# Kernel tuning notes

Hardware: AMD Instinct MI355X
Metric: run time of the kernel (lower is better)

## Reference

```python
import jax, jax.numpy as jnp
import numpy as np
from jax import lax

WS = 7            # window size
DIM = 256         # out_dim
HEADS = 8
HD = DIM // HEADS # head dim = 32
HIDDEN = 4 * DIM  # mlp hidden = 1024
IN_DIM = 512
EPS = 1e-6

def _rel_pos_index(ws):
    coords = np.stack(np.meshgrid(np.arange(ws), np.arange(ws), indexing='ij'))
    cf = coords.reshape(2, -1)
    rc = (cf[:, :, None] - cf[:, None, :]).transpose(1, 2, 0)
    rc[:, :, 0] += ws - 1
    rc[:, :, 1] += ws - 1
    rc[:, :, 0] *= 2 * ws - 1
    return rc.sum(-1)  # (N, N)

RPI = jnp.asarray(_rel_pos_index(WS))  # (49, 49) int

def _layernorm(x, g, b):
    m = jnp.mean(x, axis=-1, keepdims=True)
    v = jnp.mean(jnp.square(x - m), axis=-1, keepdims=True)
    return (x - m) * lax.rsqrt(v + EPS) * g + b

def setup_inputs() -> dict:
    key = jax.random.key(0)
    ks = jax.random.split(key, 16)
    s = 0.02
    inp = {
        'x': jax.random.normal(ks[0], (8, IN_DIM, 48, 48), jnp.float32),
        'skip_feat': jax.random.normal(ks[1], (8, DIM, 96, 96), jnp.float32),
        # ConvTranspose2d(in, out, k=2, s=2): weight (in, out, 2, 2), bias (out,)
        'up_w': jax.random.normal(ks[2], (IN_DIM, DIM, 2, 2), jnp.float32) * s,
        'up_b': jnp.zeros((DIM,), jnp.float32),
        # skip_adapter Conv2d(out, out, 1, bias=False)
        'skip_w': jax.random.normal(ks[3], (DIM, DIM, 1, 1), jnp.float32) * s,
        'gamma1': jnp.ones((DIM,), jnp.float32),
        'beta1': jnp.zeros((DIM,), jnp.float32),
        'qkv_w': jax.random.normal(ks[4], (3 * DIM, DIM), jnp.float32) * s,
        'qkv_b': jnp.zeros((3 * DIM,), jnp.float32),
        'rpb_table': jax.random.normal(ks[5], ((2 * WS - 1) ** 2, HEADS), jnp.float32) * s,
        'proj_w': jax.random.normal(ks[6], (DIM, DIM), jnp.float32) * s,
        'proj_b': jnp.zeros((DIM,), jnp.float32),
        'gamma2': jnp.ones((DIM,), jnp.float32),
        'beta2': jnp.zeros((DIM,), jnp.float32),
        'mlp_w1': jax.random.normal(ks[7], (HIDDEN, DIM), jnp.float32) * s,
        'mlp_b1': jnp.zeros((HIDDEN,), jnp.float32),
        'mlp_w2': jax.random.normal(ks[8], (DIM, HIDDEN), jnp.float32) * s,
        'mlp_b2': jnp.zeros((DIM,), jnp.float32),
    }
    return inp

def _forward(x, skip_feat, up_w, up_b, skip_w, gamma1, beta1, qkv_w, qkv_b,
             rpb_table, proj_w, proj_b, gamma2, beta2, mlp_w1, mlp_b1, mlp_w2, mlp_b2):
    B = x.shape[0]
    # ConvTranspose2d k=2 s=2 p=0 == lhs-dilated conv with spatially flipped kernel
    y = lax.conv_general_dilated(
        x, jnp.flip(up_w, (2, 3)), window_strides=(1, 1),
        padding=((1, 1), (1, 1)), lhs_dilation=(2, 2),
        dimension_numbers=('NCHW', 'IOHW', 'NCHW')) + up_b[None, :, None, None]
    shortcut = y  # (B, C, Hup, Wup)
    # skip adapter (1x1 conv, no bias); shapes match so no interpolate/adhoc conv
    y = y + jnp.einsum('oi,bihw->bohw', skip_w[:, :, 0, 0], skip_feat)
    xh = jnp.transpose(y, (0, 2, 3, 1))  # (B, H, W, C)
    H, W, C = xh.shape[1], xh.shape[2], xh.shape[3]
    xn = _layernorm(xh, gamma1, beta1)
    pad_b = (WS - H % WS) % WS
    pad_r = (WS - W % WS) % WS
    xp = jnp.pad(xn, ((0, 0), (0, pad_b), (0, pad_r), (0, 0)))
    Hp, Wp = H + pad_b, W + pad_r
    N = WS * WS
    # window partition -> (B * nWh * nWw, N, C)
    win = xp.reshape(B, Hp // WS, WS, Wp // WS, WS, C)
    win = jnp.transpose(win, (0, 1, 3, 2, 4, 5)).reshape(-1, N, C)
    B_ = win.shape[0]
    # attention
    qkv = (win @ qkv_w.T + qkv_b).reshape(B_, N, 3, HEADS, HD)
    qkv = jnp.transpose(qkv, (2, 0, 3, 1, 4))  # (3, B_, h, N, hd)
    q, k, v = qkv[0], qkv[1], qkv[2]
    attn = jnp.einsum('bhnd,bhmd->bhnm', q * (HD ** -0.5), k)
    bias = rpb_table[RPI.reshape(-1)].reshape(N, N, HEADS)
    attn = attn + jnp.transpose(bias, (2, 0, 1))[None]  # (B_, h, N, N)
    attn = jax.nn.softmax(attn, axis=-1)
    o = jnp.einsum('bhnm,bhmd->bhnd', attn, v)
    o = jnp.transpose(o, (0, 2, 1, 3)).reshape(B_, N, C)
    o = o @ proj_w.T + proj_b
    # window reverse + crop
    o = o.reshape(B, Hp // WS, Wp // WS, WS, WS, C)
    o = jnp.transpose(o, (0, 1, 3, 2, 4, 5)).reshape(B, Hp, Wp, C)[:, :H, :W]
    x2 = jnp.transpose(shortcut, (0, 2, 3, 1)) + o
    # MLP
    h = jax.nn.gelu(_layernorm(x2, gamma2, beta2) @ mlp_w1.T + mlp_b1, approximate=False)
    x3 = x2 + (h @ mlp_w2.T + mlp_b2)
    return jnp.transpose(x3, (0, 3, 1, 2))  # (B, C, Hup, Wup)

def reference(x, skip_feat, up_w, up_b, skip_w, gamma1, beta1, qkv_w, qkv_b,
              rpb_table, proj_w, proj_b, gamma2, beta2, mlp_w1, mlp_b1, mlp_w2, mlp_b2):
    return _forward(x, skip_feat, up_w, up_b, skip_w, gamma1, beta1, qkv_w, qkv_b,
                    rpb_table, proj_w, proj_b, gamma2, beta2, mlp_w1, mlp_b1, mlp_w2, mlp_b2)
```

## Files before the change

kernel.cpp:

```cpp
#include <hip/hip_runtime.h>

typedef __attribute__((ext_vector_type(8))) short short8;
typedef __attribute__((ext_vector_type(4))) float f32x4;
typedef __attribute__((ext_vector_type(4))) unsigned short u16x4;
typedef unsigned short u16;
typedef unsigned int u32;

#define DEV static __device__ __forceinline__

DEV u16 f2b(float f) {
  u32 u = __builtin_bit_cast(u32, f);
  return (u16)((u + 0x7fffu + ((u >> 16) & 1u)) >> 16);
}
DEV float b2f(u16 h) {
  u32 u = ((u32)h) << 16;
  return __builtin_bit_cast(float, u);
}
DEV short8 ld8(const u16* p) { return *reinterpret_cast<const short8*>(p); }
DEV f32x4 mfma16(short8 a, short8 b, f32x4 c) {
  return __builtin_amdgcn_mfma_f32_16x16x32_bf16(a, b, c, 0, 0, 0);
}
DEV float wredsum(float v) {
#pragma unroll
  for (int off = 1; off < 64; off <<= 1) v += __shfl_xor(v, off);
  return v;
}

#define GLL(gp, lp) __builtin_amdgcn_global_load_lds( \
    (const __attribute__((address_space(1))) void*)(gp), \
    (__attribute__((address_space(3))) void*)(lp), 16, 0, 0)

#define WQKV   0
#define WPROJ  196608
#define WM1    262144
#define WM2    524288
#define WSKIP  786432
#define WUP    851968

#define OFF_BIAS 2752512u
#define OFF_SC   2883584u
#define OFF_OVR  40632320u
#define OFF_STAT (OFF_OVR + 52000000u)
#define OFF_PST  (OFF_OVR + 52600000u)
#define OFF_SGB  (OFF_OVR + 55000000u)
#define WS_NEED  96227328u

__global__ void k_sentinel(float* out) { out[threadIdx.x] = 31337.0f; }

__global__ __launch_bounds__(256) void k_prep(
    const float* qkv_w, const float* proj_w, const float* mlp_w1,
    const float* mlp_w2, const float* skip_w, const float* up_w,
    const float* rpb, const float* g1, const float* be1,
    const float* g2, const float* be2, u16* W, float* bias_g, float* sgb) {
  int i = blockIdx.x * 256 + threadIdx.x;
  if (i < 196608) { W[WQKV + i] = f2b(qkv_w[i] * g1[i & 255]); return; }
  i -= 196608;
  if (i < 65536) { W[WPROJ + i] = f2b(proj_w[i]); return; }
  i -= 65536;
  if (i < 262144) { W[WM1 + i] = f2b(mlp_w1[i] * g2[i & 255]); return; }
  i -= 262144;
  if (i < 262144) { W[WM2 + i] = f2b(mlp_w2[i]); return; }
  i -= 262144;
  if (i < 65536) { W[WSKIP + i] = f2b(skip_w[i]); return; }
  i -= 65536;
  if (i < 524288) {
    int ci = i & 511; int rest = i >> 9; int co = rest & 255; int kk = rest >> 8;
    W[WUP + i] = f2b(up_w[ci * 1024 + co * 4 + kk]);
    return;
  }
  i -= 524288;
  if (i < 32768) {
    int h = i >> 12, r = i & 4095, ii = r >> 6, j = r & 63;
    float v;
    if (j >= 49) v = -1e30f;
    else if (ii >= 49) v = 0.f;
    else {
      int d0 = (ii / 7 - j / 7) + 6, d1 = (ii % 7 - j % 7) + 6;
      v = rpb[(d0 * 13 + d1) * 8 + h];
    }
    bias_g[i] = v;
    return;
  }
  i -= 32768;
  if (i < 1024) {
    float s = 0.f;
    for (int k = 0; k < 256; k++) s += g2[k] * mlp_w1[i * 256 + k];
    sgb[i] = s;
    return;
  }
  i -= 1024;
  if (i < 1024) {
    float s = 0.f;
    for (int k = 0; k < 256; k++) s += be2[k] * mlp_w1[i * 256 + k];
    sgb[1024 + i] = s;
    return;
  }
  i -= 1024;
  if (i < 768) {
    float s = 0.f;
    for (int k = 0; k < 256; k++) s += be1[k] * qkv_w[i * 256 + k];
    sgb[2816 + i] = s;
    return;
  }
}

__global__ __launch_bounds__(256) void k_tr(const float* src, u16* dst, int C, int HW) {
  __shared__ float t[32][33];
  int hw0 = blockIdx.x * 32, c0 = blockIdx.y * 32, b = blockIdx.z;
  int tx = threadIdx.x & 31, ty = threadIdx.x >> 5;
  const float* s = src + (size_t)b * C * HW;
  u16* d = dst + (size_t)b * C * HW;
#pragma unroll
  for (int i = 0; i < 4; i++)
    t[ty + i * 8][tx] = s[(size_t)(c0 + ty + i * 8) * HW + hw0 + tx];
  __syncthreads();
#pragma unroll
  for (int i = 0; i < 4; i++)
    d[(size_t)(hw0 + ty + i * 8) * C + c0 + tx] = f2b(t[tx][ty + i * 8]);
}

__global__ __launch_bounds__(256) void k_tr_skip(const float* src, u16* dst) {
  __shared__ float t[32][33];
  int w0 = blockIdx.x * 32, c0 = blockIdx.y * 32;
  int z = blockIdx.z;
  int b = z / 96, h = z - b * 96;
  int tx = threadIdx.x & 31, ty = threadIdx.x >> 5;
  const float* s = src + (size_t)b * 256 * 9216 + (size_t)h * 96;
  u16* d = dst + (((size_t)b * 96 + h) * 96) * 256;
#pragma unroll
  for (int i = 0; i < 4; i++)
    t[ty + i * 8][tx] = s[(size_t)(c0 + ty + i * 8) * 9216 + w0 + tx];
  __syncthreads();
#pragma unroll
  for (int i = 0; i < 4; i++)
    d[(size_t)(w0 + ty + i * 8) * 256 + c0 + tx] = f2b(t[tx][ty + i * 8]);
}

__global__ __launch_bounds__(256) void k1g(
    const u16* W, const u16* xt, const float* up_b, u16* sc) {
  __shared__ __align__(16) u16 Ab[2][4096];
  __shared__ __align__(16) u16 Bb[2][4096];
  int tid = threadIdx.x;
  int lane = tid & 63, wave = tid >> 6;
  int m = lane & 15, gq = lane >> 4;
  int wr = wave >> 1, wc = wave & 1;
  int bm = blockIdx.x * 128, bn = blockIdx.y * 128;
  int kk = blockIdx.z, kh = kk >> 1, kw = kk & 1;
  const u16* Ag = xt + (size_t)bm * 512;
  const u16* Bg = W + WUP + (size_t)kk * 131072 + (size_t)bn * 512;
  f32x4 acc[4][4] = {};
#pragma unroll
  for (int c = 0; c < 2; c++) {
    int flat = (wave * 2 + c) * 512 + lane * 8;
    int r = flat >> 5, cc = flat & 31;
    GLL(Ag + (size_t)r * 512 + cc, &Ab[0][(wave * 2 + c) * 512]);
    GLL(Bg + (size_t)r * 512 + cc, &Bb[0][(wave * 2 + c) * 512]);
  }
  __syncthreads();
  int cur = 0;
  for (int ki = 0; ki < 16; ki++) {
    if (ki < 15) {
      int kkk = (ki + 1) * 32;
#pragma unroll
      for (int c = 0; c < 2; c++) {
        int flat = (wave * 2 + c) * 512 + lane * 8;
        int r = flat >> 5, cc = flat & 31;
        GLL(Ag + (size_t)r * 512 + kkk + cc, &Ab[cur ^ 1][(wave * 2 + c) * 512]);
        GLL(Bg + (size_t)r * 512 + kkk + cc, &Bb[cur ^ 1][(wave * 2 + c) * 512]);
      }
    }
    short8 aF[4], bF[4];
#pragma unroll
    for (int mt = 0; mt < 4; mt++)
      aF[mt] = ld8(&Ab[cur][(wr * 64 + mt * 16 + m) * 32 + gq * 8]);
#pragma unroll
    for (int nt = 0; nt < 4; nt++)
      bF[nt] = ld8(&Bb[cur][(wc * 64 + nt * 16 + m) * 32 + gq * 8]);
#pragma unroll
    for (int mt = 0; mt < 4; mt++)
#pragma unroll
      for (int nt = 0; nt < 4; nt++)
        acc[mt][nt] = mfma16(aF[mt], bF[nt], acc[mt][nt]);
    __syncthreads();
    cur ^= 1;
  }
  float ub[4];
#pragma unroll
  for (int nt = 0; nt < 4; nt++) ub[nt] = up_b[bn + wc * 64 + nt * 16 + m];
#pragma unroll
  for (int mt = 0; mt < 4; mt++)
#pragma unroll
    for (int rr = 0; rr < 4; rr++) {
      int t = bm + wr * 64 + mt * 16 + gq * 4 + rr;
      int b = t / 2304, rem = t - b * 2304;
      int ih = rem / 48, iw = rem - ih * 48;
      int h = 2 * ih + kh, w = 2 * iw + kw;
      size_t tok = ((size_t)b * 96 + h) * 96 + w;
#pragma unroll
      for (int nt = 0; nt < 4; nt++) {
        int ch = bn + wc * 64 + nt * 16 + m;
        sc[tok * 256 + ch] = f2b(acc[mt][nt][rr] + ub[nt]);
      }
    }
}

__global__ __launch_bounds__(256) void k2y(
    const u16* W, const u16* skt, const u16* sc, u16* ybuf, float* pstat) {
  __shared__ __align__(16) u16 Ab[2][4096];
  __shared__ __align__(16) u16 Bb[2][4096];
  int tid = threadIdx.x;
  int lane = tid & 63, wave = tid >> 6;
  int m = lane & 15, gq = lane >> 4;
  int wr = wave >> 1, wc = wave & 1;
  int bm = blockIdx.x * 128, bn = blockIdx.y * 128;
  const u16* Ag = skt + (size_t)bm * 256;
  const u16* Bg = W + WSKIP + (size_t)bn * 256;
  f32x4 acc[4][4] = {};
#pragma unroll
  for (int c = 0; c < 2; c++) {
    int flat = (wave * 2 + c) * 512 + lane * 8;
    int r = flat >> 5, cc = flat & 31;
    GLL(Ag + (size_t)r * 256 + cc, &Ab[0][(wave * 2 + c) * 512]);
    GLL(Bg + (size_t)r * 256 + cc, &Bb[0][(wave * 2 + c) * 512]);
  }
  __syncthreads();
  int cur = 0;
  for (int ki = 0; ki < 8; ki++) {
    if (ki < 7) {
      int kk = (ki + 1) * 32;
#pragma unroll
      for (int c = 0; c < 2; c++) {
        int flat = (wave * 2 + c) * 512 + lane * 8;
        int r = flat >> 5, cc = flat & 31;
        GLL(Ag + (size_t)r * 256 + kk + cc, &Ab[cur ^ 1][(wave * 2 + c) * 512]);
        GLL(Bg + (size_t)r * 256 + kk + cc, &Bb[cur ^ 1][(wave * 2 + c) * 512]);
      }
    }
    short8 aF[4], bF[4];
#pragma unroll
    for (int mt = 0; mt < 4; mt++)
      aF[mt] = ld8(&Ab[cur][(wr * 64 + mt * 16 + m) * 32 + gq * 8]);
#pragma unroll
    for (int nt = 0; nt < 4; nt++)
      bF[nt] = ld8(&Bb[cur][(wc * 64 + nt * 16 + m) * 32 + gq * 8]);
#pragma unroll
    for (int mt = 0; mt < 4; mt++)
#pragma unroll
      for (int nt = 0; nt < 4; nt++)
        acc[mt][nt] = mfma16(aF[mt], bF[nt], acc[mt][nt]);
    __syncthreads();
    cur ^= 1;
  }
#pragma unroll
  for (int mt = 0; mt < 4; mt++)
#pragma unroll
    for (int rr = 0; rr < 4; rr++) {
      int tok = bm + wr * 64 + mt * 16 + gq * 4 + rr;
      float s = 0.f, s2 = 0.f;
#pragma unroll
      for (int nt = 0; nt < 4; nt++) {
        int ch = bn + wc * 64 + nt * 16 + m;
        float y = acc[mt][nt][rr] + b2f(sc[(size_t)tok * 256 + ch]);
        ybuf[(size_t)tok * 256 + ch] = f2b(y);
        s += y; s2 += y * y;
      }
#pragma unroll
      for (int off = 1; off < 16; off <<= 1) {
        s += __shfl_xor(s, off);
        s2 += __shfl_xor(s2, off);
      }
      if (m == 0) {
        int pi = (tok * 4 + blockIdx.y * 2 + wc) * 2;
        pstat[pi] = s;
        pstat[pi + 1] = s2;
      }
    }
}

__global__ __launch_bounds__(256) void k_statfin(const float* pstat, float* stat) {
  int row = blockIdx.x * 256 + threadIdx.x;
  float s = 0.f, s2 = 0.f;
#pragma unroll
  for (int j = 0; j < 4; j++) {
    s += pstat[(row * 4 + j) * 2];
    s2 += pstat[(row * 4 + j) * 2 + 1];
  }
  float mean = s * 0.00390625f;
  float var = s2 * 0.00390625f - mean * mean;
  float r = rsqrtf(var + 1e-6f);
  stat[row * 2] = r;
  stat[row * 2 + 1] = r * mean;
}

__global__ __launch_bounds__(256) void k23(
    const u16* W, const u16* ybuf, const float* stat, const float* sgb,
    const float* qkv_b, const float* bias_g, u16* obr) {
  __shared__ __align__(16) u16 yl[52 * 264];
  __shared__ __align__(16) u16 pws[4][6144];
  int tid = threadIdx.x;
  int lane = tid & 63, wave = tid >> 6;
  int m = lane & 15, gq = lane >> 4, k0 = gq * 8;
  int blk = blockIdx.x;
  int bimg = blk / 196, wl = blk - bimg * 196;
  int wrow = wl / 14, wcol = wl - wrow * 14;
  int h0 = wrow * 7, w0 = wcol * 7;
  u16* prv = pws[wave];
#pragma unroll
  for (int t = 0; t < 8; t++) {
    u16x4 z = {};
    *reinterpret_cast<u16x4*>(&prv[t * 256 + lane * 4]) = z;
  }
  for (int it = 0; it < 7; it++) {
    int flat = it * 256 + tid;
    if (flat < 1568) {
      int row = flat >> 5, cc = (flat & 31) * 8;
      int hh = h0 + row / 7, ww = w0 + row % 7;
      short8 v = {};
      if (hh < 96 && ww < 96) {
        int ras = (bimg * 96 + hh) * 96 + ww;
        short8 raw = ld8(ybuf + (size_t)ras * 256 + cc);
        float rs = stat[ras * 2], rmu = stat[ras * 2 + 1];
#pragma unroll
        for (int q2 = 0; q2 < 8; q2++) {
          float zz = b2f(((const u16*)&raw)[q2]) * rs - rmu;
          ((u16*)&v)[q2] = f2b(zz);
        }
      }
      *reinterpret_cast<short8*>(&yl[row * 264 + cc]) = v;
    }
  }
  __syncthreads();
  const float scale = 0.1767766952966369f;
#pragma unroll
  for (int hp = 0; hp < 2; hp++) {
    int h = wave * 2 + hp;
    {
      f32x4 acc[4][6] = {};
#pragma unroll 2
      for (int ks = 0; ks < 8; ks++) {
        short8 a[4];
#pragma unroll
        for (int mt = 0; mt < 4; mt++) {
          int row = mt * 16 + m; if (row > 48) row = 48;
          a[mt] = ld8(&yl[row * 264 + ks * 32 + k0]);
        }
#pragma unroll
        for (int nt = 0; nt < 6; nt++) {
          int brow = (nt >> 1) * 256 + h * 32 + (nt & 1) * 16 + m;
          short8 bb = ld8(W + WQKV + (size_t)brow * 256 + ks * 32 + k0);
#pragma unroll
          for (int mt = 0; mt < 4; mt++)
            acc[mt][nt] = mfma16(a[mt], bb, acc[mt][nt]);
        }
      }
      float qb_[6], sb1[6];
      int hdv[6];
#pragma unroll
      for (int nt = 0; nt < 6; nt++) {
        int hd = (nt & 1) * 16 + m;
        int c = (nt >> 1) * 256 + h * 32 + hd;
        qb_[nt] = qkv_b[c];
        sb1[nt] = sgb[2816 + c];
        hdv[nt] = hd;
      }
#pragma unroll
      for (int mt = 0; mt < 4; mt++)
#pragma unroll
        for (int rr = 0; rr < 4; rr++) {
          int row = mt * 16 + gq * 4 + rr;
          if (row >= 49) continue;
          int hh = h0 + row / 7, ww = w0 + row % 7;
          float vf = (hh < 96 && ww < 96) ? 1.f : 0.f;
#pragma unroll
          for (int nt = 0; nt < 6; nt++) {
            u16 val = f2b(acc[mt][nt][rr] + vf * sb1[nt] + qb_[nt]);
            if ((nt >> 1) == 0) prv[2048 + row * 32 + hdv[nt]] = val;
            else if ((nt >> 1) == 1) prv[3616 + row * 32 + hdv[nt]] = val;
            else prv[hdv[nt] * 64 + row] = val;
          }
        }
    }
    short8 aq[4], bk[4];
#pragma unroll
    for (int mt = 0; mt < 4; mt++) { int i = mt * 16 + m; if (i > 48) i = 48; aq[mt] = ld8(&prv[2048 + i * 32 + k0]); }
#pragma unroll
    for (int nt = 0; nt < 4; nt++) { int j = nt * 16 + m; if (j > 48) j = 48; bk[nt] = ld8(&prv[3616 + j * 32 + k0]); }
    f32x4 s[4][4] = {};
#pragma unroll
    for (int mt = 0; mt < 4; mt++)
#pragma unroll
      for (int nt = 0; nt < 4; nt++)
        s[mt][nt] = mfma16(aq[mt], bk[nt], s[mt][nt]);
    const float* BI = bias_g + h * 4096;
    float rsum[4][4];
#pragma unroll
    for (int mt = 0; mt < 4; mt++)
#pragma unroll
      for (int rr = 0; rr < 4; rr++) {
        int i = mt * 16 + gq * 4 + rr;
        float sv[4];
        float mx = -1e38f;
#pragma unroll
        for (int nt = 0; nt < 4; nt++) {
          sv[nt] = s[mt][nt][rr] * scale + BI[i * 64 + nt * 16 + m];
          mx = fmaxf(mx, sv[nt]);
        }
        mx = fmaxf(mx, __shfl_xor(mx, 1));
        mx = fmaxf(mx, __shfl_xor(mx, 2));
        mx = fmaxf(mx, __shfl_xor(mx, 4));
        mx = fmaxf(mx, __shfl_xor(mx, 8));
        float sum = 0.f;
#pragma unroll
        for (int nt = 0; nt < 4; nt++) { sv[nt] = __expf(sv[nt] - mx); sum += sv[nt]; }
        sum += __shfl_xor(sum, 1);
        sum += __shfl_xor(sum, 2);
        sum += __shfl_xor(sum, 4);
        sum += __shfl_xor(sum, 8);
        rsum[mt][rr] = sum;
        int isw = (i & 7) * 8;
#pragma unroll
        for (int nt = 0; nt < 4; nt++) {
          int j = nt * 16 + m;
          prv[2048 + i * 64 + (j ^ isw)] = f2b(sv[nt]);
        }
      }
    f32x4 o[4][2] = {};
#pragma unroll
    for (int ks = 0; ks < 2; ks++) {
      short8 bv[2];
#pragma unroll
      for (int nt = 0; nt < 2; nt++)
        bv[nt] = ld8(&prv[(nt * 16 + m) * 64 + ks * 32 + k0]);
#pragma unroll
      for (int mt = 0; mt < 4; mt++) {
        int i = mt * 16 + m;
        short8 ap = *reinterpret_cast<const short8*>(
            &prv[2048 + i * 64 + ((ks * 32 + k0) ^ ((i & 7) * 8))]);
#pragma unroll
        for (int nt = 0; nt < 2; nt++)
          o[mt][nt] = mfma16(ap, bv[nt], o[mt][nt]);
      }
    }
#pragma unroll
    for (int mt = 0; mt < 4; mt++)
#pragma unroll
      for (int rr = 0; rr < 4; rr++) {
        int i = mt * 16 + gq * 4 + rr;
        if (i >= 49) continue;
        int hh = h0 + i / 7, ww = w0 + i % 7;
        if (hh >= 96 || ww >= 96) continue;
        size_t ras = ((size_t)bimg * 96 + hh) * 96 + ww;
        float rinv = 1.f / rsum[mt][rr];
#pragma unroll
        for (int nt = 0; nt < 2; nt++) {
          int c = h * 32 + nt * 16 + m;
          obr[ras * 256 + c] = f2b(o[mt][nt][rr] * rinv);
        }
      }
  }
}

__global__ __launch_bounds__(256) void k4r(
    const u16* W, const u16* obr, const float* proj_b, u16* sc, float* pstat) {
  __shared__ __align__(16) u16 Ab[2][4096];
  __shared__ __align__(16) u16 Bb[2][4096];
  int tid = threadIdx.x;
  int lane = tid & 63, wave = tid >> 6;
  int m = lane & 15, gq = lane >> 4;
  int wr = wave >> 1, wc = wave & 1;
  int bm = blockIdx.x * 128, bn = blockIdx.y * 128;
  const u16* Ag = obr + (size_t)bm * 256;
  const u16* Bg = W + WPROJ + (size_t)bn * 256;
  f32x4 acc[4][4] = {};
#pragma unroll
  for (int c = 0; c < 2; c++) {
    int flat = (wave * 2 + c) * 512 + lane * 8;
    int r = flat >> 5, cc = flat & 31;
    GLL(Ag + (size_t)r * 256 + cc, &Ab[0][(wave * 2 + c) * 512]);
    GLL(Bg + (size_t)r * 256 + cc, &Bb[0][(wave * 2 + c) * 512]);
  }
  __syncthreads();
  int cur = 0;
  for (int ki = 0; ki < 8; ki++) {
    if (ki < 7) {
      int kk = (ki + 1) * 32;
#pragma unroll
      for (int c = 0; c < 2; c++) {
        int flat = (wave * 2 + c) * 512 + lane * 8;
        int r = flat >> 5, cc = flat & 31;
        GLL(Ag + (size_t)r * 256 + kk + cc, &Ab[cur ^ 1][(wave * 2 + c) * 512]);
        GLL(Bg + (size_t)r * 256 + kk + cc, &Bb[cur ^ 1][(wave * 2 + c) * 512]);
      }
    }
    short8 aF[4], bF[4];
#pragma unroll
    for (int mt = 0; mt < 4; mt++)
      aF[mt] = ld8(&Ab[cur][(wr * 64 + mt * 16 + m) * 32 + gq * 8]);
#pragma unroll
    for (int nt = 0; nt < 4; nt++)
      bF[nt] = ld8(&Bb[cur][(wc * 64 + nt * 16 + m) * 32 + gq * 8]);
#pragma unroll
    for (int mt = 0; mt < 4; mt++)
#pragma unroll
      for (int nt = 0; nt < 4; nt++)
        acc[mt][nt] = mfma16(aF[mt], bF[nt], acc[mt][nt]);
    __syncthreads();
    cur ^= 1;
  }
#pragma unroll
  for (int mt = 0; mt < 4; mt++)
#pragma unroll
    for (int rr = 0; rr < 4; rr++) {
      int tok = bm + wr * 64 + mt * 16 + gq * 4 + rr;
      float s = 0.f, s2 = 0.f;
#pragma unroll
      for (int nt = 0; nt < 4; nt++) {
        int ch = bn + wc * 64 + nt * 16 + m;
        float v = acc[mt][nt][rr] + proj_b[ch] + b2f(sc[(size_t)tok * 256 + ch]);
        sc[(size_t)tok * 256 + ch] = f2b(v);
        s += v; s2 += v * v;
      }
#pragma unroll
      for (int off = 1; off < 16; off <<= 1) {
        s += __shfl_xor(s, off);
        s2 += __shfl_xor(s2, off);
      }
      if (m == 0) {
        int pi = (tok * 4 + blockIdx.y * 2 + wc) * 2;
        pstat[pi] = s;
        pstat[pi + 1] = s2;
      }
    }
}

__global__ __launch_bounds__(256) void k5f(
    const u16* W, const u16* x2b, const float* stat, const float* sgb,
    const float* mb1, u16* h1q) {
  __shared__ __align__(16) u16 Ab[2][4096];
  __shared__ __align__(16) u16 Bb[2][4096];
  int tid = threadIdx.x;
  int lane = tid & 63, wave = tid >> 6;
  int m = lane & 15, gq = lane >> 4;
  int wr = wave >> 1, wc = wave & 1;
  int bm = blockIdx.x * 128, bn = blockIdx.y * 128;
  const u16* Ag = x2b + (size_t)bm * 256;
  const u16* Bg = W + WM1 + (size_t)bn * 256;
  f32x4 acc[4][4] = {};
#pragma unroll
  for (int c = 0; c < 2; c++) {
    int flat = (wave * 2 + c) * 512 + lane * 8;
    int r = flat >> 5, cc = flat & 31;
    GLL(Ag + (size_t)r * 256 + cc, &Ab[0][(wave * 2 + c) * 512]);
    GLL(Bg + (size_t)r * 256 + cc, &Bb[0][(wave * 2 + c) * 512]);
  }
  __syncthreads();
  int cur = 0;
  for (int ki = 0; ki < 8; ki++) {
    if (ki < 7) {
      int kk = (ki + 1) * 32;
#pragma unroll
      for (int c = 0; c < 2; c++) {
        int flat = (wave * 2 + c) * 512 + lane * 8;
        int r = flat >> 5, cc = flat & 31;
        GLL(Ag + (size_t)r * 256 + kk + cc, &Ab[cur ^ 1][(wave * 2 + c) * 512]);
        GLL(Bg + (size_t)r * 256 + kk + cc, &Bb[cur ^ 1][(wave * 2 + c) * 512]);
      }
    }
    short8 aF[4], bF[4];
#pragma unroll
    for (int mt = 0; mt < 4; mt++)
      aF[mt] = ld8(&Ab[cur][(wr * 64 + mt * 16 + m) * 32 + gq * 8]);
#pragma unroll
    for (int nt = 0; nt < 4; nt++)
      bF[nt] = ld8(&Bb[cur][(wc * 64 + nt * 16 + m) * 32 + gq * 8]);
#pragma unroll
    for (int mt = 0; mt < 4; mt++)
#pragma unroll
      for (int nt = 0; nt < 4; nt++)
        acc[mt][nt] = mfma16(aF[mt], bF[nt], acc[mt][nt]);
    __syncthreads();
    cur ^= 1;
  }
  float sgv[4], sbv[4], b1v[4];
#pragma unroll
  for (int nt = 0; nt < 4; nt++) {
    int ch = bn + wc * 64 + nt * 16 + m;
    sgv[nt] = sgb[ch];
    sbv[nt] = sgb[1024 + ch];
    b1v[nt] = mb1[ch];
  }
#pragma unroll
  for (int mt = 0; mt < 4; mt++)
#pragma unroll
    for (int rr = 0; rr < 4; rr++) {
      int tok = bm + wr * 64 + mt * 16 + gq * 4 + rr;
      float rs = stat[tok * 2], rmu = stat[tok * 2 + 1];
#pragma unroll
      for (int nt = 0; nt < 4; nt++) {
        float v = rs * acc[mt][nt][rr] - rmu * sgv[nt] + sbv[nt] + b1v[nt];
        v = 0.5f * v * (1.f + erff(v * 0.7071067811865475f));
        h1q[(size_t)tok * 1024 + (bn + wc * 64 + nt * 16 + m)] = f2b(v);
      }
    }
}

__global__ __launch_bounds__(256) void k6g(
    const u16* W, const u16* h1q, const float* mb2, const u16* x2b,
    float* out, int tok_base) {
  __shared__ __align__(16) u16 Ab[2][2048];
  __shared__ __align__(16) u16 Bb[2][4096];
  __shared__ float ot[128 * 66];
  int tid = threadIdx.x;
  int lane = tid & 63, wave = tid >> 6;
  int m = lane & 15, gq = lane >> 4;
  int wr = wave >> 1, wc = wave & 1;
  int bm = blockIdx.x * 64, bn = blockIdx.y * 128;
  const u16* Ag = h1q + (size_t)bm * 1024;
  const u16* Bg = W + WM2 + (size_t)bn * 1024;
  f32x4 acc[2][4] = {};
  {
    int flatA = wave * 512 + lane * 8;
    GLL(Ag + (size_t)(flatA >> 5) * 1024 + (flatA & 31), &Ab[0][wave * 512]);
#pragma unroll
    for (int c = 0; c < 2; c++) {
      int flat = (wave * 2 + c) * 512 + lane * 8;
      GLL(Bg + (size_t)(flat >> 5) * 1024 + (flat & 31), &Bb[0][(wave * 2 + c) * 512]);
    }
  }
  __syncthreads();
  int cur = 0;
  for (int ki = 0; ki < 32; ki++) {
    if (ki < 31) {
      int kk = (ki + 1) * 32;
      int flatA = wave * 512 + lane * 8;
      GLL(Ag + (size_t)(flatA >> 5) * 1024 + kk + (flatA & 31), &Ab[cur ^ 1][wave * 512]);
#pragma unroll
      for (int c = 0; c < 2; c++) {
        int flat = (wave * 2 + c) * 512 + lane * 8;
        GLL(Bg + (size_t)(flat >> 5) * 1024 + kk + (flat & 31), &Bb[cur ^ 1][(wave * 2 + c) * 512]);
      }
    }
    short8 aF[2], bF[4];
#pragma unroll
    for (int mt = 0; mt < 2; mt++)
      aF[mt] = ld8(&Ab[cur][(wr * 32 + mt * 16 + m) * 32 + gq * 8]);
#pragma unroll
    for (int nt = 0; nt < 4; nt++)
      bF[nt] = ld8(&Bb[cur][(wc * 64 + nt * 16 + m) * 32 + gq * 8]);
#pragma unroll
    for (int mt = 0; mt < 2; mt++)
#pragma unroll
      for (int nt = 0; nt < 4; nt++)
        acc[mt][nt] = mfma16(aF[mt], bF[nt], acc[mt][nt]);
    __syncthreads();
    cur ^= 1;
  }
#pragma unroll
  for (int nt = 0; nt < 4; nt++) {
    int nl = wc * 64 + nt * 16 + m;
    int ch = bn + nl;
    float bias = mb2[ch];
#pragma unroll
    for (int mt = 0; mt < 2; mt++)
#pragma unroll
      for (int rr = 0; rr < 4; rr++) {
        int tl = wr * 32 + mt * 16 + gq * 4 + rr;
        float v = acc[mt][nt][rr] + bias + b2f(x2b[(size_t)(bm + tl) * 256 + ch]);
        ot[nl * 66 + tl] = v;
      }
  }
  __syncthreads();
  int tg = tok_base + bm;
  int bimg = tg / 9216, hw0 = tg % 9216;
  for (int it = 0; it < 32; it++) {
    int flat = it * 256 + tid;
    int j = flat >> 6, t = flat & 63;
    out[((size_t)bimg * 256 + bn + j) * 9216 + hw0 + t] = ot[j * 66 + t];
  }
}

extern "C" void kernel_launch(void* const* d_in, const int* in_sizes, int n_in,
                              void* d_out, int out_size, void* d_ws, size_t ws_size,
                              hipStream_t stream) {
  const float* x      = (const float*)d_in[0];
  const float* skipf  = (const float*)d_in[1];
  const float* up_w   = (const float*)d_in[2];
  const float* up_b   = (const float*)d_in[3];
  const float* skip_w = (const float*)d_in[4];
  const float* g1     = (const float*)d_in[5];
  const float* be1    = (const float*)d_in[6];
  const float* qkv_w  = (const float*)d_in[7];
  const float* qkv_b  = (const float*)d_in[8];
  const float* rpb    = (const float*)d_in[9];
  const float* proj_w = (const float*)d_in[10];
  const float* proj_b = (const float*)d_in[11];
  const float* g2     = (const float*)d_in[12];
  const float* be2    = (const float*)d_in[13];
  const float* m_w1   = (const float*)d_in[14];
  const float* m_b1   = (const float*)d_in[15];
  const float* m_w2   = (const float*)d_in[16];
  const float* m_b2   = (const float*)d_in[17];
  if (ws_size < WS_NEED) {
    k_sentinel<<<1, 256, 0, stream>>>((float*)d_out);
    return;
  }
  char* ws = (char*)d_ws;
  u16*   W    = (u16*)ws;
  float* bias = (float*)(ws + OFF_BIAS);
  u16*   sc   = (u16*)(ws + OFF_SC);
  u16*   xt   = (u16*)(ws + OFF_OVR);
  u16*   skt  = (u16*)(ws + OFF_OVR);
  u16*   h1q  = (u16*)(ws + OFF_OVR);
  float* stat = (float*)(ws + OFF_STAT);
  float* pst  = (float*)(ws + OFF_PST);
  float* sgb  = (float*)(ws + OFF_SGB);
  u16*   ybuf = (u16*)d_out;
  u16*   obr  = (u16*)((char*)d_out + 37748736u);

  k_prep<<<5519, 256, 0, stream>>>(qkv_w, proj_w, m_w1, m_w2, skip_w, up_w, rpb,
                                   g1, be1, g2, be2, W, bias, sgb);
  k_tr<<<dim3(72, 16, 8), 256, 0, stream>>>(x, xt, 512, 2304);
  k1g<<<dim3(144, 2, 4), 256, 0, stream>>>(W, xt, up_b, sc);
  k_tr_skip<<<dim3(3, 8, 768), 256, 0, stream>>>(skipf, skt);
  k2y<<<dim3(576, 2), 256, 0, stream>>>(W, skt, sc, ybuf, pst);
  k_statfin<<<288, 256, 0, stream>>>(pst, stat);
  k23<<<1568, 256, 0, stream>>>(W, ybuf, stat, sgb, qkv_b, bias, obr);
  k4r<<<dim3(576, 2), 256, 0, stream>>>(W, obr, proj_b, sc, pst);
  k_statfin<<<288, 256, 0, stream>>>(pst, stat);
  for (int q = 0; q < 4; q++) {
    const u16* x2b = sc + (size_t)q * 18432 * 256;
    k5f<<<dim3(144, 8), 256, 0, stream>>>(W, x2b, stat + (size_t)q * 36864,
                                          sgb, m_b1, h1q);
    k6g<<<dim3(288, 2), 256, 0, stream>>>(W, h1q, m_b2, x2b, (float*)d_out, q * 18432);
  }
}
```

Before: 665.8 us.

## Keep V in registers via shuffles and shrink attention LDS for higher occupancy

The fused QKV+attention kernel now computes V in a separate MFMA pass and keeps it in registers. The B operand for the P·V product is built with cross-lane shuffles rather than stored transposed in LDS. This shrinks the per-wave scratch and the input tile, dropping LDS from about 75KB to about 50KB per block, and adds a launch bound of 3 blocks per SM to raise occupancy. It also drops the scratch zero-init and guards the padded probability rows. The cost is reloading the yl tile for a second GEMM pass, many shuffles, and register pressure under the tighter launch bound.

```diff
diff --git a/kernel.cpp b/kernel.cpp
--- a/kernel.cpp
+++ b/kernel.cpp
@@ -292,11 +292,11 @@
   stat[row * 2 + 1] = r * mean;
 }
 
-__global__ __launch_bounds__(256) void k23(
+__global__ __launch_bounds__(256, 3) void k23(
     const u16* W, const u16* ybuf, const float* stat, const float* sgb,
     const float* qkv_b, const float* bias_g, u16* obr) {
-  __shared__ __align__(16) u16 yl[52 * 264];
-  __shared__ __align__(16) u16 pws[4][6144];
+  __shared__ __align__(16) u16 yl[49 * 264];
+  __shared__ __align__(16) u16 pws[4][3136];
   int tid = threadIdx.x;
   int lane = tid & 63, wave = tid >> 6;
   int m = lane & 15, gq = lane >> 4, k0 = gq * 8;
@@ -305,11 +305,8 @@
   int wrow = wl / 14, wcol = wl - wrow * 14;
   int h0 = wrow * 7, w0 = wcol * 7;
   u16* prv = pws[wave];
-#pragma unroll
-  for (int t = 0; t < 8; t++) {
-    u16x4 z = {};
-    *reinterpret_cast<u16x4*>(&prv[t * 256 + lane * 4]) = z;
-  }
+  int slo = (2 * (gq & 1)) * 16 + m;
+  int shi = slo + 16;
   for (int it = 0; it < 7; it++) {
     int flat = it * 256 + tid;
     if (flat < 1568) {
@@ -335,7 +332,7 @@
   for (int hp = 0; hp < 2; hp++) {
     int h = wave * 2 + hp;
     {
-      f32x4 acc[4][6] = {};
+      f32x4 acc[4][4] = {};
 #pragma unroll 2
       for (int ks = 0; ks < 8; ks++) {
         short8 a[4];
@@ -345,7 +342,7 @@
           a[mt] = ld8(&yl[row * 264 + ks * 32 + k0]);
         }
 #pragma unroll
-        for (int nt = 0; nt < 6; nt++) {
+        for (int nt = 0; nt < 4; nt++) {
           int brow = (nt >> 1) * 256 + h * 32 + (nt & 1) * 16 + m;
           short8 bb = ld8(W + WQKV + (size_t)brow * 256 + ks * 32 + k0);
 #pragma unroll
@@ -353,38 +350,72 @@
             acc[mt][nt] = mfma16(a[mt], bb, acc[mt][nt]);
         }
       }
-      float qb_[6], sb1[6];
-      int hdv[6];
-#pragma unroll
-      for (int nt = 0; nt < 6; nt++) {
+#pragma unroll
+      for (int nt = 0; nt < 4; nt++) {
         int hd = (nt & 1) * 16 + m;
         int c = (nt >> 1) * 256 + h * 32 + hd;
-        qb_[nt] = qkv_b[c];
-        sb1[nt] = sgb[2816 + c];
-        hdv[nt] = hd;
+        float qb_ = qkv_b[c];
+        float sb1 = sgb[2816 + c];
+#pragma unroll
+        for (int mt = 0; mt < 4; mt++)
+#pragma unroll
+          for (int rr = 0; rr < 4; rr++) {
+            int row = mt * 16 + gq * 4 + rr;
+            if (row >= 49) continue;
+            int hh = h0 + row / 7, ww = w0 + row % 7;
+            float vf = (hh < 96 && ww < 96) ? 1.f : 0.f;
+            u16 val = f2b(acc[mt][nt][rr] + vf * sb1 + qb_);
+            if (nt < 2) prv[row * 32 + hd] = val;
+            else prv[1568 + row * 32 + hd] = val;
+          }
+      }
+    }
+    f32x4 vacc[4][2] = {};
+    {
+#pragma unroll 2
+      for (int ks = 0; ks < 8; ks++) {
+        short8 a[4];
+#pragma unroll
+        for (int mt = 0; mt < 4; mt++) {
+          int row = mt * 16 + m; if (row > 48) row = 48;
+          a[mt] = ld8(&yl[row * 264 + ks * 32 + k0]);
+        }
+#pragma unroll
+        for (int nv = 0; nv < 2; nv++) {
+          int brow = 512 + h * 32 + nv * 16 + m;
+          short8 bb = ld8(W + WQKV + (size_t)brow * 256 + ks * 32 + k0);
+#pragma unroll
+          for (int mt = 0; mt < 4; mt++)
+            vacc[mt][nv] = mfma16(a[mt], bb, vacc[mt][nv]);
+        }
+      }
+      float qbv[2], sbv[2];
+#pragma unroll
+      for (int nv = 0; nv < 2; nv++) {
+        int c = 512 + h * 32 + nv * 16 + m;
+        qbv[nv] = qkv_b[c];
+        sbv[nv] = sgb[2816 + c];
       }
 #pragma unroll
       for (int mt = 0; mt < 4; mt++)
 #pragma unroll
         for (int rr = 0; rr < 4; rr++) {
           int row = mt * 16 + gq * 4 + rr;
-          if (row >= 49) continue;
-          int hh = h0 + row / 7, ww = w0 + row % 7;
-          float vf = (hh < 96 && ww < 96) ? 1.f : 0.f;
-#pragma unroll
-          for (int nt = 0; nt < 6; nt++) {
-            u16 val = f2b(acc[mt][nt][rr] + vf * sb1[nt] + qb_[nt]);
-            if ((nt >> 1) == 0) prv[2048 + row * 32 + hdv[nt]] = val;
-            else if ((nt >> 1) == 1) prv[3616 + row * 32 + hdv[nt]] = val;
-            else prv[hdv[nt] * 64 + row] = val;
+          float vf = 0.f;
+          if (row < 49) {
+            int hh = h0 + row / 7, ww = w0 + row % 7;
+            vf = (hh < 96 && ww < 96) ? 1.f : 0.f;
           }
+#pragma unroll
+          for (int nv = 0; nv < 2; nv++)
+            vacc[mt][nv][rr] += vf * sbv[nv] + qbv[nv];
         }
     }
     short8 aq[4], bk[4];
 #pragma unroll
-    for (int mt = 0; mt < 4; mt++) { int i = mt * 16 + m; if (i > 48) i = 48; aq[mt] = ld8(&prv[2048 + i * 32 + k0]); }
-#pragma unroll
-    for (int nt = 0; nt < 4; nt++) { int j = nt * 16 + m; if (j > 48) j = 48; bk[nt] = ld8(&prv[3616 + j * 32 + k0]); }
+    for (int mt = 0; mt < 4; mt++) { int i = mt * 16 + m; if (i > 48) i = 48; aq[mt] = ld8(&prv[i * 32 + k0]); }
+#pragma unroll
+    for (int nt = 0; nt < 4; nt++) { int j = nt * 16 + m; if (j > 48) j = 48; bk[nt] = ld8(&prv[1568 + j * 32 + k0]); }
     f32x4 s[4][4] = {};
 #pragma unroll
     for (int mt = 0; mt < 4; mt++)
@@ -417,11 +448,13 @@
         sum += __shfl_xor(sum, 4);
         sum += __shfl_xor(sum, 8);
         rsum[mt][rr] = sum;
-        int isw = (i & 7) * 8;
-#pragma unroll
-        for (int nt = 0; nt < 4; nt++) {
-          int j = nt * 16 + m;
-          prv[2048 + i * 64 + (j ^ isw)] = f2b(sv[nt]);
+        if (i < 49) {
+          int isw = (i & 7) * 8;
+#pragma unroll
+          for (int nt = 0; nt < 4; nt++) {
+            int j = nt * 16 + m;
+            prv[i * 64 + (j ^ isw)] = f2b(sv[nt]);
+          }
         }
       }
     f32x4 o[4][2] = {};
@@ -429,16 +462,27 @@
     for (int ks = 0; ks < 2; ks++) {
       short8 bv[2];
 #pragma unroll
-      for (int nt = 0; nt < 2; nt++)
-        bv[nt] = ld8(&prv[(nt * 16 + m) * 64 + ks * 32 + k0]);
+      for (int nv = 0; nv < 2; nv++) {
+        u16 tmp[8];
+#pragma unroll
+        for (int rr = 0; rr < 4; rr++) {
+          float a0 = __shfl(vacc[2 * ks][nv][rr], slo);
+          float a1 = __shfl(vacc[2 * ks + 1][nv][rr], slo);
+          tmp[rr] = f2b((gq & 2) ? a1 : a0);
+          float b0 = __shfl(vacc[2 * ks][nv][rr], shi);
+          float b1 = __shfl(vacc[2 * ks + 1][nv][rr], shi);
+          tmp[4 + rr] = f2b((gq & 2) ? b1 : b0);
+        }
+        bv[nv] = *reinterpret_cast<const short8*>(tmp);
+      }
 #pragma unroll
       for (int mt = 0; mt < 4; mt++) {
-        int i = mt * 16 + m;
+        int i = mt * 16 + m; if (i > 48) i = 48;
         short8 ap = *reinterpret_cast<const short8*>(
-            &prv[2048 + i * 64 + ((ks * 32 + k0) ^ ((i & 7) * 8))]);
-#pragma unroll
-        for (int nt = 0; nt < 2; nt++)
-          o[mt][nt] = mfma16(ap, bv[nt], o[mt][nt]);
+            &prv[i * 64 + ((ks * 32 + k0) ^ ((i & 7) * 8))]);
+#pragma unroll
+        for (int nv = 0; nv < 2; nv++)
+          o[mt][nv] = mfma16(ap, bv[nv], o[mt][nv]);
       }
     }
 #pragma unroll
@@ -452,9 +496,9 @@
         size_t ras = ((size_t)bimg * 96 + hh) * 96 + ww;
         float rinv = 1.f / rsum[mt][rr];
 #pragma unroll
-        for (int nt = 0; nt < 2; nt++) {
-          int c = h * 32 + nt * 16 + m;
-          obr[ras * 256 + c] = f2b(o[mt][nt][rr] * rinv);
+        for (int nv = 0; nv < 2; nv++) {
+          int c = h * 32 + nv * 16 + m;
+          obr[ras * 256 + c] = f2b(o[mt][nv][rr] * rinv);
         }
       }
   }
```

After: 736.5 us. 1.11x slower.
